# Kernel tuning notes

Hardware: AMD Instinct MI355X
Metric: run time of the kernel (lower is better)

## Reference

```python
import jax, jax.numpy as jnp
import numpy as np

NS, T, N = 32, 2048, 1024
DT, TAU = 0.1, 1.0


def setup_inputs() -> dict:
    key = jax.random.key(0)
    k1, k2, k3 = jax.random.split(key, 3)
    std = 0.2 / np.sqrt(N)
    inp = jax.random.normal(k1, (NS, T, N), dtype=jnp.float32)
    A = (jax.random.normal(k2, (N, N), dtype=jnp.float32) * std)
    h0 = (jax.random.normal(k3, (NS, N), dtype=jnp.float32) * std)
    return {"inp": inp, "A": A, "h0": h0}


def reference(inp, A, h0):
    # Leaky RNN with phi = identity, signature=None (J = A), noise_std = 0.
    # h_{t+1} = (1 - dt/tau) h_t + (dt/tau) (h_t @ A^T + u_t)
    alpha = DT / TAU

    def step(h, x_t):
        h_new = (1.0 - alpha) * h + alpha * (h @ A.T + x_t)
        return h_new, h_new  # rates[t] = phi(h) = h

    xs = jnp.swapaxes(inp[:, : T - 1, :], 0, 1)  # [T-1, NS, N] time-major
    _, hs = jax.lax.scan(step, h0, xs)           # hs: [T-1, NS, N]
    rates = jnp.concatenate([h0[None], hs], axis=0)  # rates[0] = phi(h0)
    return jnp.swapaxes(rates, 0, 1)             # [NS, T, N]
```

## Files before the change

kernel.cpp:

```cpp
#include <hip/hip_runtime.h>
#include <hip/hip_bf16.h>


#define NSAMP 32
#define TSTEPS 2048
#define NDIM 1024
#define CHUNK_L 8
#define WARM 128
#define NCHUNK (TSTEPS / CHUNK_L)
#define HS_STRIDE 1544

typedef __attribute__((ext_vector_type(8))) short short8;
typedef __attribute__((ext_vector_type(4))) float floatx4;

__global__ __launch_bounds__(256)
void prep_A_kernel(const float* __restrict__ A, __hip_bfloat16* __restrict__ Bp) {
    int idx = blockIdx.x * 256 + threadIdx.x;
    int k  = idx & (NDIM - 1);
    int n  = idx >> 10;
    int kt = k >> 5, kk = k & 31;
    Bp[((kt << 10) + n) * 32 + kk] = __float2bfloat16(A[idx]);
}

__global__ __launch_bounds__(512, 2)
void rnn_chunk_kernel(const float* __restrict__ inp,
                      const float* __restrict__ h0,
                      const __hip_bfloat16* __restrict__ Bp,
                      float* __restrict__ out) {
    __shared__ __hip_bfloat16 Hs[NSAMP * HS_STRIDE];

    const int c    = blockIdx.x;
    const int tid  = threadIdx.x;
    const int lane = tid & 63;
    const int wave = tid >> 6;
    const int q    = lane >> 4;
    const int m16  = lane & 15;

    const int out_lo  = c * CHUNK_L;
    const int out_hi  = out_lo + CHUNK_L;
    const int t_start = (out_lo > WARM) ? (out_lo - WARM) : 0;

    float hreg[2][8][4];

    #pragma unroll
    for (int mt = 0; mt < 2; ++mt)
    #pragma unroll
    for (int j = 0; j < 8; ++j) {
        const int n = (wave * 8 + j) * 16 + m16;
        #pragma unroll
        for (int r = 0; r < 4; ++r) {
            const int s = mt * 16 + q * 4 + r;
            const float h = (t_start == 0) ? h0[s * NDIM + n] : 0.0f;
            hreg[mt][j][r] = h;
            Hs[s * HS_STRIDE + n] = __float2bfloat16(h);
            if (c == 0) out[((size_t)s * TSTEPS) * NDIM + n] = h;
        }
    }
    __syncthreads();

    for (int t = t_start + 1; t < out_hi; ++t) {
        floatx4 acc[2][8] = {};

        for (int kt = 0; kt < 32; ++kt) {
            const short8 a0 = *(const short8*)&Hs[(m16     ) * HS_STRIDE + kt * 32 + q * 8];
            const short8 a1 = *(const short8*)&Hs[(m16 + 16) * HS_STRIDE + kt * 32 + q * 8];
            #pragma unroll
            for (int j = 0; j < 8; ++j) {
                const short8 b = *(const short8*)&Bp[(size_t)(kt * NDIM + (wave * 8 + j) * 16 + m16) * 32 + q * 8];
                acc[0][j] = __builtin_amdgcn_mfma_f32_16x16x32_bf16(a0, b, acc[0][j], 0, 0, 0);
                acc[1][j] = __builtin_amdgcn_mfma_f32_16x16x32_bf16(a1, b, acc[1][j], 0, 0, 0);
            }
        }

        __syncthreads();

        const bool emit = (t >= out_lo);
        #pragma unroll
        for (int mt = 0; mt < 2; ++mt)
        #pragma unroll
        for (int j = 0; j < 8; ++j) {
            const int n = (wave * 8 + j) * 16 + m16;
            #pragma unroll
            for (int r = 0; r < 4; ++r) {
                const int s = mt * 16 + q * 4 + r;
                const float x = inp[((size_t)s * TSTEPS + (t - 1)) * NDIM + n];
                const float h = 0.9f * hreg[mt][j][r] + 0.1f * (acc[mt][j][r] + x);
                hreg[mt][j][r] = h;
                Hs[s * HS_STRIDE + n] = __float2bfloat16(h);
                if (emit) out[((size_t)s * TSTEPS + t) * NDIM + n] = h;
            }
        }
        __syncthreads();
    }
}

extern "C" void kernel_launch(void* const* d_in, const int* in_sizes, int n_in,
                              void* d_out, int out_size, void* d_ws, size_t ws_size,
                              hipStream_t stream) {
    const float* inp = (const float*)d_in[0];
    const float* A   = (const float*)d_in[1];
    const float* h0  = (const float*)d_in[2];
    float* out = (float*)d_out;
    __hip_bfloat16* Bp = (__hip_bfloat16*)d_ws;

    hipLaunchKernelGGL(prep_A_kernel, dim3((NDIM * NDIM) / 256), dim3(256), 0, stream, A, Bp);
    hipLaunchKernelGGL(rnn_chunk_kernel, dim3(NCHUNK), dim3(512), 0, stream, inp, h0, Bp, out);
}
```

Measured before the change: 7.606 ms.

## Double chunk length, use 1024-thread blocks and software-prefetch A tiles

Doubles the output chunk per block, which halves the block count and cuts the total redundant warm-up recurrence work. Each block now runs 16 waves, each owning 64 output columns, so each CU has more waves to hide latency. The k-loop is fully unrolled and double-buffers the bf16 A fragments from global memory, and the LDS row stride is changed. The trade-offs: only half as many blocks occupy the GPU, and the tighter launch bounds may force register spills.

```diff
diff --git a/kernel.cpp b/kernel.cpp
--- a/kernel.cpp
+++ b/kernel.cpp
@@ -2,13 +2,12 @@
 #include <hip/hip_bf16.h>
 
 
-#define NSAMP 32
 #define TSTEPS 2048
 #define NDIM 1024
-#define CHUNK_L 8
+#define CHUNK_L 16
 #define WARM 128
 #define NCHUNK (TSTEPS / CHUNK_L)
-#define HS_STRIDE 1544
+#define HS 1288
 
 typedef __attribute__((ext_vector_type(8))) short short8;
 typedef __attribute__((ext_vector_type(4))) float floatx4;
@@ -22,12 +21,12 @@
     Bp[((kt << 10) + n) * 32 + kk] = __float2bfloat16(A[idx]);
 }
 
-__global__ __launch_bounds__(512, 2)
+__global__ __launch_bounds__(1024, 4)
 void rnn_chunk_kernel(const float* __restrict__ inp,
                       const float* __restrict__ h0,
                       const __hip_bfloat16* __restrict__ Bp,
                       float* __restrict__ out) {
-    __shared__ __hip_bfloat16 Hs[NSAMP * HS_STRIDE];
+    __shared__ __hip_bfloat16 Hs[32 * HS];
 
     const int c    = blockIdx.x;
     const int tid  = threadIdx.x;
@@ -40,36 +39,51 @@
     const int out_hi  = out_lo + CHUNK_L;
     const int t_start = (out_lo > WARM) ? (out_lo - WARM) : 0;
 
-    float hreg[2][8][4];
+    float hreg[2][4][4];
 
     #pragma unroll
     for (int mt = 0; mt < 2; ++mt)
     #pragma unroll
-    for (int j = 0; j < 8; ++j) {
-        const int n = (wave * 8 + j) * 16 + m16;
+    for (int j = 0; j < 4; ++j) {
+        const int n = wave * 64 + j * 16 + m16;
         #pragma unroll
         for (int r = 0; r < 4; ++r) {
             const int s = mt * 16 + q * 4 + r;
             const float h = (t_start == 0) ? h0[s * NDIM + n] : 0.0f;
             hreg[mt][j][r] = h;
-            Hs[s * HS_STRIDE + n] = __float2bfloat16(h);
+            Hs[s * HS + n] = __float2bfloat16(h);
             if (c == 0) out[((size_t)s * TSTEPS) * NDIM + n] = h;
         }
     }
     __syncthreads();
 
+    const __hip_bfloat16* const bbase = Bp + ((size_t)(wave * 64 + m16) * 32 + q * 8);
+
     for (int t = t_start + 1; t < out_hi; ++t) {
-        floatx4 acc[2][8] = {};
+        floatx4 acc[2][4] = {};
+        const __hip_bfloat16* bp = bbase;
 
+        short8 bcur[4], bnxt[4];
+        #pragma unroll
+        for (int j = 0; j < 4; ++j) bcur[j] = *(const short8*)(bp + j * 512);
+
+        #pragma unroll
         for (int kt = 0; kt < 32; ++kt) {
-            const short8 a0 = *(const short8*)&Hs[(m16     ) * HS_STRIDE + kt * 32 + q * 8];
-            const short8 a1 = *(const short8*)&Hs[(m16 + 16) * HS_STRIDE + kt * 32 + q * 8];
+            const short8 a0 = *(const short8*)&Hs[ m16       * HS + kt * 32 + q * 8];
+            const short8 a1 = *(const short8*)&Hs[(m16 + 16) * HS + kt * 32 + q * 8];
+            if (kt < 31) {
+                const __hip_bfloat16* bn = bp + 32768;
+                #pragma unroll
+                for (int j = 0; j < 4; ++j) bnxt[j] = *(const short8*)(bn + j * 512);
+                bp = bn;
+            }
             #pragma unroll
-            for (int j = 0; j < 8; ++j) {
-                const short8 b = *(const short8*)&Bp[(size_t)(kt * NDIM + (wave * 8 + j) * 16 + m16) * 32 + q * 8];
-                acc[0][j] = __builtin_amdgcn_mfma_f32_16x16x32_bf16(a0, b, acc[0][j], 0, 0, 0);
-                acc[1][j] = __builtin_amdgcn_mfma_f32_16x16x32_bf16(a1, b, acc[1][j], 0, 0, 0);
+            for (int j = 0; j < 4; ++j) {
+                acc[0][j] = __builtin_amdgcn_mfma_f32_16x16x32_bf16(a0, bcur[j], acc[0][j], 0, 0, 0);
+                acc[1][j] = __builtin_amdgcn_mfma_f32_16x16x32_bf16(a1, bcur[j], acc[1][j], 0, 0, 0);
             }
+            #pragma unroll
+            for (int j = 0; j < 4; ++j) bcur[j] = bnxt[j];
         }
 
         __syncthreads();
@@ -78,15 +92,15 @@
         #pragma unroll
         for (int mt = 0; mt < 2; ++mt)
         #pragma unroll
-        for (int j = 0; j < 8; ++j) {
-            const int n = (wave * 8 + j) * 16 + m16;
+        for (int j = 0; j < 4; ++j) {
+            const int n = wave * 64 + j * 16 + m16;
             #pragma unroll
             for (int r = 0; r < 4; ++r) {
                 const int s = mt * 16 + q * 4 + r;
                 const float x = inp[((size_t)s * TSTEPS + (t - 1)) * NDIM + n];
                 const float h = 0.9f * hreg[mt][j][r] + 0.1f * (acc[mt][j][r] + x);
                 hreg[mt][j][r] = h;
-                Hs[s * HS_STRIDE + n] = __float2bfloat16(h);
+                Hs[s * HS + n] = __float2bfloat16(h);
                 if (emit) out[((size_t)s * TSTEPS + t) * NDIM + n] = h;
             }
         }
@@ -104,5 +118,5 @@
     __hip_bfloat16* Bp = (__hip_bfloat16*)d_ws;
 
     hipLaunchKernelGGL(prep_A_kernel, dim3((NDIM * NDIM) / 256), dim3(256), 0, stream, A, Bp);
-    hipLaunchKernelGGL(rnn_chunk_kernel, dim3(NCHUNK), dim3(512), 0, stream, inp, h0, Bp, out);
+    hipLaunchKernelGGL(rnn_chunk_kernel, dim3(NCHUNK), dim3(1024), 0, stream, inp, h0, Bp, out);
 }
```

Measured after the change: 13.88 ms. 82.5% more time.
